# Performance work log

Measured on AMD Instinct MI355X. Metric: run time of the kernel, lower is better.

## Reference

```python
import jax, jax.numpy as jnp
import numpy as np

N = 50000       # nodes
E = 800000      # edges (before self-loops)
IN_DIM = 256
HIDDEN = 256
HEADS = 4
C1 = HIDDEN // HEADS  # 64 per-head channels in layer 1
OUT_DIM = 128
NEG_SLOPE = 0.2  # PyG GATConv default negative_slope


def setup_inputs() -> dict:
    key = jax.random.key(0)
    ks = jax.random.split(key, 10)
    x = jax.random.normal(ks[0], (N, IN_DIM), dtype=jnp.float32) * 0.1
    edge_index = jax.random.randint(ks[1], (2, E), 0, N, dtype=jnp.int64)
    # layer 1 params (GATConv: lin weight, att_src, att_dst, bias)
    W1 = jax.random.normal(ks[2], (IN_DIM, HEADS * C1), dtype=jnp.float32) * 0.05
    att_src1 = jax.random.normal(ks[3], (HEADS, C1), dtype=jnp.float32) * 0.05
    att_dst1 = jax.random.normal(ks[4], (HEADS, C1), dtype=jnp.float32) * 0.05
    bias1 = jnp.zeros((HEADS * C1,), dtype=jnp.float32)
    # layer 2 params (heads=1, concat=False)
    W2 = jax.random.normal(ks[5], (HIDDEN, OUT_DIM), dtype=jnp.float32) * 0.05
    att_src2 = jax.random.normal(ks[6], (1, OUT_DIM), dtype=jnp.float32) * 0.05
    att_dst2 = jax.random.normal(ks[7], (1, OUT_DIM), dtype=jnp.float32) * 0.05
    bias2 = jnp.zeros((OUT_DIM,), dtype=jnp.float32)
    return {"x": x, "edge_index": edge_index, "W1": W1, "att_src1": att_src1,
            "att_dst1": att_dst1, "bias1": bias1, "W2": W2, "att_src2": att_src2,
            "att_dst2": att_dst2, "bias2": bias2}


def gat_conv(x, src, dst, W, a_src, a_dst, bias, concat):
    # x: [N, F_in]; src/dst: [E'] (self-loops included); W: [F_in, H*C]
    H, C = a_src.shape
    h = (x @ W).reshape(-1, H, C)                      # [N, H, C]
    alpha_s = (h * a_src[None]).sum(-1)                # [N, H]
    alpha_d = (h * a_dst[None]).sum(-1)                # [N, H]
    e = jax.nn.leaky_relu(alpha_s[src] + alpha_d[dst], NEG_SLOPE)  # [E', H]
    # segment softmax over incoming edges of each destination node
    emax = jax.ops.segment_max(e, dst, num_segments=N)             # [N, H]
    ex = jnp.exp(e - emax[dst])
    denom = jax.ops.segment_sum(ex, dst, num_segments=N)           # [N, H]
    alpha = ex / (denom[dst] + 1e-16)                              # [E', H]
    msg = h[src] * alpha[:, :, None]                               # [E', H, C]
    out = jax.ops.segment_sum(msg, dst, num_segments=N)            # [N, H, C]
    if concat:
        out = out.reshape(N, H * C)
    else:
        out = out.mean(axis=1)
    return out + bias


def reference(x, edge_index, W1, att_src1, att_dst1, bias1, W2, att_src2, att_dst2, bias2):
    # PyG GATConv add_self_loops=True
    loops = jnp.arange(N, dtype=edge_index.dtype)
    src = jnp.concatenate([edge_index[0], loops])
    dst = jnp.concatenate([edge_index[1], loops])
    h = gat_conv(x, src, dst, W1, att_src1, att_dst1, bias1, concat=True)   # [N, 256]
    h = jax.nn.gelu(h, approximate=False)  # torch F.gelu default = exact erf
    # dropout inactive in eval mode
    out = gat_conv(h, src, dst, W2, att_src2, att_dst2, bias2, concat=False)  # [N, 128]
    return out
```

## Files before the change

### kernel.cpp

```cpp
#include <hip/hip_runtime.h>
#include <hip/hip_bf16.h>


#define IN_DIM   256
#define HID      256
#define HEADS    4
#define C1       64
#define OUT_DIM  128
#define NEG_SLOPE 0.2f

using short8 = __attribute__((ext_vector_type(8))) short;
using f32x4  = __attribute__((ext_vector_type(4))) float;

__device__ __forceinline__ float loadf(const void* p, size_t i, int isbf16) {
    return isbf16 ? __bfloat162float(((const __hip_bfloat16*)p)[i])
                  : ((const float*)p)[i];
}

__device__ __forceinline__ float leaky(float a) {
    return a > 0.f ? a : NEG_SLOPE * a;
}

__device__ __forceinline__ unsigned short f2bs(float f) {
    __hip_bfloat16 b = __float2bfloat16(f);
    return *reinterpret_cast<unsigned short*>(&b);
}

__device__ __forceinline__ float blo(unsigned u) {
    return __uint_as_float(u << 16);
}
__device__ __forceinline__ float bhi(unsigned u) {
    return __uint_as_float(u & 0xffff0000u);
}

__device__ __forceinline__ float gelu(float c) {
    return 0.5f * c * (1.0f + erff(c * 0.70710678f));
}


__global__ void prep_tpose_kernel(const void* x, int nx,
                                  const void* W1, const void* as1w, const void* ad1w,
                                  const void* b1, const void* W2, const void* as2w,
                                  const void* ad2w, const void* b2,
                                  float* as1wf, float* ad1wf, float* b1f,
                                  float* as2wf, float* ad2wf, float* b2f,
                                  int* flags,
                                  __hip_bfloat16* __restrict__ W1T,
                                  __hip_bfloat16* __restrict__ W2T,
                                  int* __restrict__ deg, int n) {
    __shared__ int red[4];
    __shared__ int flagS;
    int b = blockIdx.x;
    int t = threadIdx.x;

    if (b < 9) {
        const void* srcs[9] = {x, W1, as1w, ad1w, b1, W2, as2w, ad2w, b2};
        int ns[9] = {nx, IN_DIM * HID, HEADS * C1, HEADS * C1, HID,
                     HID * OUT_DIM, OUT_DIM, OUT_DIM, OUT_DIM};
        float* dsts[9] = {nullptr, nullptr, as1wf, ad1wf, b1f, nullptr, as2wf, ad2wf, b2f};

        const unsigned short* u = (const unsigned short*)srcs[b];
        int nn = ns[b];
        int nslots = nn < 4096 ? nn : 4096;
        int cnt = 0;
        for (int i = t; i < nslots; i += 256) {
            unsigned short a = u[i] & 0x7FFF;
            int e = a >> 7;
            if (a == 0 || (e >= 90 && e <= 140)) cnt++;
        }
        for (int o = 32; o > 0; o >>= 1) cnt += __shfl_down(cnt, o);
        if ((t & 63) == 0) red[t >> 6] = cnt;
        __syncthreads();
        if (t == 0) {
            int tot = red[0] + red[1] + red[2] + red[3];
            int f = (tot * 10 >= nslots * 8) ? 1 : 0;
            flags[b] = f;
            flagS = f;
        }
        __syncthreads();
        int f = flagS;
        float* d = dsts[b];
        if (d) {
            for (int i = t; i < nn; i += 256) d[i] = loadf(srcs[b], i, f);
        }
        return;
    }

    int bb = b - 9;
    int gi = bb * 256 + t;
    if (gi < n) deg[gi] = 0;

    const void* src = (bb < 256) ? W1 : W2;
    const unsigned short* u = (const unsigned short*)src;
    int cnt = 0;
    for (int i = t; i < 4096; i += 256) {
        unsigned short a = u[i] & 0x7FFF;
        int e = a >> 7;
        if (a == 0 || (e >= 90 && e <= 140)) cnt++;
    }
    for (int o = 32; o > 0; o >>= 1) cnt += __shfl_down(cnt, o);
    if ((t & 63) == 0) red[t >> 6] = cnt;
    __syncthreads();
    if (t == 0) flagS = ((red[0] + red[1] + red[2] + red[3]) * 10 >= 4096 * 8) ? 1 : 0;
    __syncthreads();
    int f = flagS;

    if (bb < 256) {
        int i = bb * 256 + t;
        int k = i >> 8, nn = i & 255;
        W1T[nn * 256 + k] = __float2bfloat16(loadf(W1, i, f));
    } else {
        int i = (bb - 256) * 256 + t;
        int k = i >> 7, nn = i & 127;
        W2T[nn * 256 + k] = __float2bfloat16(loadf(W2, i, f));
    }
}


__global__ void count_kernel(const int* __restrict__ ei, int E, int EP,
                             int* __restrict__ deg, int* __restrict__ pos) {
    int idx = blockIdx.x * blockDim.x + threadIdx.x;
    if (idx >= EP) return;
    int d = (idx < E) ? ei[E + idx] : (idx - E);
    pos[idx] = atomicAdd(&deg[d], 1);
}

__global__ __launch_bounds__(256) void psum_kernel(const int* __restrict__ deg,
                                                   int* __restrict__ bsum, int n) {
    int i = blockIdx.x * 256 + threadIdx.x;
    int v = (i < n) ? deg[i] : 0;
#pragma unroll
    for (int o = 32; o > 0; o >>= 1) v += __shfl_down(v, o);
    __shared__ int red[4];
    if ((threadIdx.x & 63) == 0) red[threadIdx.x >> 6] = v;
    __syncthreads();
    if (threadIdx.x == 0) bsum[blockIdx.x] = red[0] + red[1] + red[2] + red[3];
}

__global__ __launch_bounds__(256) void wscan_kernel(const int* __restrict__ deg,
                                                    const int* __restrict__ bsum,
                                                    int* __restrict__ offs,
                                                    float* __restrict__ z0,
                                                    float* __restrict__ z1,
                                                    int n) {
    __shared__ int sh[256];
    __shared__ int red[4];
    int b = blockIdx.x;
    int t = threadIdx.x;

    int pref = (t < b) ? bsum[t] : 0;
#pragma unroll
    for (int o = 32; o > 0; o >>= 1) pref += __shfl_down(pref, o);
    if ((t & 63) == 0) red[t >> 6] = pref;
    __syncthreads();
    int bpref = red[0] + red[1] + red[2] + red[3];

    int i = b * 256 + t;
    int v = (i < n) ? deg[i] : 0;
    sh[t] = v;
    __syncthreads();
    for (int d = 1; d < 256; d <<= 1) {
        int u = (t >= d) ? sh[t - d] : 0;
        __syncthreads();
        sh[t] += u;
        __syncthreads();
    }
    int excl = sh[t] - v + bpref;
    if (i < n) {
        offs[i] = excl;
        z0[i] = 0.f;
        z1[i] = 0.f;
        if (i == n - 1) offs[n] = excl + v;
    }
}

__global__ void fill_kernel(const int* __restrict__ ei, int E, int EP,
                            const int* __restrict__ offs,
                            const int* __restrict__ pos,
                            int* __restrict__ ssrc) {
    int idx = blockIdx.x * blockDim.x + threadIdx.x;
    if (idx >= EP) return;
    int src = (idx < E) ? ei[idx]     : (idx - E);
    int dst = (idx < E) ? ei[E + idx] : (idx - E);
    ssrc[offs[dst] + pos[idx]] = src;
}


__device__ __forceinline__ void store_out(float* C, size_t i, float v) { C[i] = v; }
__device__ __forceinline__ void store_out(__hip_bfloat16* C, size_t i, float v) {
    C[i] = __float2bfloat16(v);
}

template <typename OutT>
__global__ __launch_bounds__(256) void gemm_mfma(
    const void* __restrict__ A0, const int* aflagp,
    const __hip_bfloat16* __restrict__ BT,
    OutT* __restrict__ C, int M, int Nn, int K,
    const float* __restrict__ aswp, const float* __restrict__ adwp,
    float* __restrict__ asO, float* __restrict__ adO, int hstride) {
    constexpr int BM = 128, BN = 128, BK = 32;
    constexpr int LDK = BK + 8;
    __shared__ __hip_bfloat16 As[BM * LDK];
    __shared__ __hip_bfloat16 Bs[BN * LDK];

    const int Mb = (M + BM - 1) / BM;
    const int Nb = Nn / BN;
    int bmi, bni;
    if (Nb == 2) {
        int L = blockIdx.x;
        bmi = (L >> 4) * 8 + (L & 7);
        bni = (L >> 3) & 1;
        if (bmi >= Mb) return;
    } else {
        bmi = blockIdx.x;
        bni = 0;
        if (bmi >= Mb) return;
    }

    const int aflag = aflagp ? *aflagp : 1;
    const int tid  = threadIdx.x;
    const int lane = tid & 63;
    const int wv   = tid >> 6;
    const int wm   = (wv >> 1) * 64;
    const int wn   = (wv & 1) * 64;
    const int l15  = lane & 15;
    const int quad = lane >> 4;

    const int bm = bmi * BM;
    const int bn = bni * BN;

    f32x4 acc[4][4] = {};

    for (int k0 = 0; k0 < K; k0 += BK) {
#pragma unroll
        for (int i = 0; i < 2; ++i) {
            int c    = tid + i * 256;
            int row  = c >> 2;
            int koff = (c & 3) * 8;
            int grow = bm + row;
            short8 av = {};
            if (grow < M) {
                if (aflag) {
                    av = *(const short8*)((const __hip_bfloat16*)A0 +
                                          (size_t)grow * K + k0 + koff);
                } else {
                    const float* ap = (const float*)A0 + (size_t)grow * K + k0 + koff;
                    float4 f0 = *(const float4*)ap;
                    float4 f1 = *(const float4*)(ap + 4);
                    av[0] = (short)f2bs(f0.x); av[1] = (short)f2bs(f0.y);
                    av[2] = (short)f2bs(f0.z); av[3] = (short)f2bs(f0.w);
                    av[4] = (short)f2bs(f1.x); av[5] = (short)f2bs(f1.y);
                    av[6] = (short)f2bs(f1.z); av[7] = (short)f2bs(f1.w);
                }
            }
            *(short8*)&As[row * LDK + koff] = av;
            short8 bv = *(const short8*)(BT + (size_t)(bn + row) * K + k0 + koff);
            *(short8*)&Bs[row * LDK + koff] = bv;
        }
        __syncthreads();

        short8 af[4], bf[4];
#pragma unroll
        for (int f = 0; f < 4; ++f) {
            af[f] = *(const short8*)&As[(wm + f * 16 + l15) * LDK + quad * 8];
            bf[f] = *(const short8*)&Bs[(wn + f * 16 + l15) * LDK + quad * 8];
        }
#pragma unroll
        for (int fm = 0; fm < 4; ++fm)
#pragma unroll
            for (int fn = 0; fn < 4; ++fn)
                acc[fm][fn] = __builtin_amdgcn_mfma_f32_16x16x32_bf16(
                    af[fm], bf[fn], acc[fm][fn], 0, 0, 0);
        __syncthreads();
    }

#pragma unroll
    for (int fm = 0; fm < 4; ++fm) {
#pragma unroll
        for (int r = 0; r < 4; ++r) {
            int grow = bm + wm + fm * 16 + quad * 4 + r;
            if (grow >= M) continue;
#pragma unroll
            for (int fn = 0; fn < 4; ++fn) {
                int gcol = bn + wn + fn * 16 + l15;
                store_out(C, (size_t)grow * Nn + gcol, acc[fm][fn][r]);
            }
        }
    }

    if (aswp) {
        float aw[4], dw[4];
#pragma unroll
        for (int fn = 0; fn < 4; ++fn) {
            int gcol = bn + wn + fn * 16 + l15;
            aw[fn] = aswp[gcol];
            dw[fn] = adwp[gcol];
        }
        int head = (bn + wn) >> 6;
#pragma unroll
        for (int fm = 0; fm < 4; ++fm) {
#pragma unroll
            for (int r = 0; r < 4; ++r) {
                int grow = bm + wm + fm * 16 + quad * 4 + r;
                float sa = acc[fm][0][r] * aw[0] + acc[fm][1][r] * aw[1]
                         + acc[fm][2][r] * aw[2] + acc[fm][3][r] * aw[3];
                float sd = acc[fm][0][r] * dw[0] + acc[fm][1][r] * dw[1]
                         + acc[fm][2][r] * dw[2] + acc[fm][3][r] * dw[3];
#pragma unroll
                for (int o = 8; o > 0; o >>= 1) {
                    sa += __shfl_xor(sa, o);
                    sd += __shfl_xor(sd, o);
                }
                if (l15 == 0 && grow < M) {
                    if (hstride == 4) {
                        asO[grow * 4 + head] = sa;
                        adO[grow * 4 + head] = sd;
                    } else {
                        atomicAdd(&asO[grow], sa);
                        atomicAdd(&adO[grow], sd);
                    }
                }
            }
        }
    }
}


__global__ __launch_bounds__(256) void agg1g_kernel(
    const uint4* __restrict__ h1, const float* __restrict__ as1,
    const float* __restrict__ ad1, const int* __restrict__ offs,
    const int* __restrict__ ssrc, const float* __restrict__ bias1,
    uint4* __restrict__ g, int n) {
    int lane = threadIdx.x & 63;
    int wv   = threadIdx.x >> 6;
    int half = lane >> 5;
    int l32  = lane & 31;
    int v = blockIdx.x * 8 + wv * 2 + half;
    if (v >= n) return;
    int head = l32 >> 3;
    int start = offs[v], end = offs[v + 1];
    float adv = ad1[v * 4 + head];

    float aL0=0,aH0=0,aL1=0,aH1=0,aL2=0,aH2=0,aL3=0,aH3=0,den=0;
    int i = start;
    for (; i + 8 <= end; i += 8) {
        int s[8];
#pragma unroll
        for (int j = 0; j < 8; ++j) s[j] = ssrc[i + j];
        float e[8]; uint4 p[8];
#pragma unroll
        for (int j = 0; j < 8; ++j) {
            e[j] = as1[s[j] * 4 + head];
            p[j] = h1[(size_t)s[j] * 32 + l32];
        }
        float w[8];
#pragma unroll
        for (int j = 0; j < 8; ++j) {
            w[j] = __expf(leaky(e[j] + adv));
            den += w[j];
        }
#pragma unroll
        for (int j = 0; j < 8; ++j) {
            aL0 = fmaf(w[j], blo(p[j].x), aL0); aH0 = fmaf(w[j], bhi(p[j].x), aH0);
            aL1 = fmaf(w[j], blo(p[j].y), aL1); aH1 = fmaf(w[j], bhi(p[j].y), aH1);
            aL2 = fmaf(w[j], blo(p[j].z), aL2); aH2 = fmaf(w[j], bhi(p[j].z), aH2);
            aL3 = fmaf(w[j], blo(p[j].w), aL3); aH3 = fmaf(w[j], bhi(p[j].w), aH3);
        }
    }
    for (; i + 4 <= end; i += 4) {
        int s0 = ssrc[i], s1 = ssrc[i+1], s2 = ssrc[i+2], s3 = ssrc[i+3];
        float e0 = as1[s0*4+head], e1 = as1[s1*4+head];
        float e2 = as1[s2*4+head], e3 = as1[s3*4+head];
        uint4 p0 = h1[(size_t)s0*32 + l32];
        uint4 p1 = h1[(size_t)s1*32 + l32];
        uint4 p2 = h1[(size_t)s2*32 + l32];
        uint4 p3 = h1[(size_t)s3*32 + l32];
        float w0 = __expf(leaky(e0+adv));
        float w1 = __expf(leaky(e1+adv));
        float w2 = __expf(leaky(e2+adv));
        float w3 = __expf(leaky(e3+adv));
        den += (w0+w1)+(w2+w3);
        aL0 = fmaf(w0, blo(p0.x), fmaf(w1, blo(p1.x), fmaf(w2, blo(p2.x), fmaf(w3, blo(p3.x), aL0))));
        aH0 = fmaf(w0, bhi(p0.x), fmaf(w1, bhi(p1.x), fmaf(w2, bhi(p2.x), fmaf(w3, bhi(p3.x), aH0))));
        aL1 = fmaf(w0, blo(p0.y), fmaf(w1, blo(p1.y), fmaf(w2, blo(p2.y), fmaf(w3, blo(p3.y), aL1))));
        aH1 = fmaf(w0, bhi(p0.y), fmaf(w1, bhi(p1.y), fmaf(w2, bhi(p2.y), fmaf(w3, bhi(p3.y), aH1))));
        aL2 = fmaf(w0, blo(p0.z), fmaf(w1, blo(p1.z), fmaf(w2, blo(p2.z), fmaf(w3, blo(p3.z), aL2))));
        aH2 = fmaf(w0, bhi(p0.z), fmaf(w1, bhi(p1.z), fmaf(w2, bhi(p2.z), fmaf(w3, bhi(p3.z), aH2))));
        aL3 = fmaf(w0, blo(p0.w), fmaf(w1, blo(p1.w), fmaf(w2, blo(p2.w), fmaf(w3, blo(p3.w), aL3))));
        aH3 = fmaf(w0, bhi(p0.w), fmaf(w1, bhi(p1.w), fmaf(w2, bhi(p2.w), fmaf(w3, bhi(p3.w), aH3))));
    }
    for (; i < end; ++i) {
        int s = ssrc[i];
        float w = __expf(leaky(as1[s*4+head] + adv));
        uint4 p = h1[(size_t)s*32 + l32];
        den += w;
        aL0 = fmaf(w, blo(p.x), aL0); aH0 = fmaf(w, bhi(p.x), aH0);
        aL1 = fmaf(w, blo(p.y), aL1); aH1 = fmaf(w, bhi(p.y), aH1);
        aL2 = fmaf(w, blo(p.z), aL2); aH2 = fmaf(w, bhi(p.z), aH2);
        aL3 = fmaf(w, blo(p.w), aL3); aH3 = fmaf(w, bhi(p.w), aH3);
    }
    float inv = 1.f / (den + 1e-16f);
    float4 bq0 = *(const float4*)&bias1[8 * l32];
    float4 bq1 = *(const float4*)&bias1[8 * l32 + 4];
    float c0 = gelu(aL0*inv + bq0.x), c1 = gelu(aH0*inv + bq0.y);
    float c2 = gelu(aL1*inv + bq0.z), c3 = gelu(aH1*inv + bq0.w);
    float c4 = gelu(aL2*inv + bq1.x), c5 = gelu(aH2*inv + bq1.y);
    float c6 = gelu(aL3*inv + bq1.z), c7 = gelu(aH3*inv + bq1.w);
    uint4 r;
    r.x = (unsigned)f2bs(c0) | ((unsigned)f2bs(c1) << 16);
    r.y = (unsigned)f2bs(c2) | ((unsigned)f2bs(c3) << 16);
    r.z = (unsigned)f2bs(c4) | ((unsigned)f2bs(c5) << 16);
    r.w = (unsigned)f2bs(c6) | ((unsigned)f2bs(c7) << 16);
    g[(size_t)v * 32 + l32] = r;
}

__global__ __launch_bounds__(256) void agg2s_kernel(
    const uint4* __restrict__ h2, const float* __restrict__ as2,
    const float* __restrict__ ad2, const int* __restrict__ offs,
    const int* __restrict__ ssrc, const float* __restrict__ bias2,
    void* __restrict__ out, const int* outflagp, int n) {
    int lane = threadIdx.x & 63;
    int wv   = threadIdx.x >> 6;
    int sub  = lane >> 4;
    int l16  = lane & 15;
    int v = blockIdx.x * 16 + wv * 4 + sub;
    if (v >= n) return;
    int start = offs[v], end = offs[v + 1];
    float adv = ad2[v];

    float a0=0,a1=0,a2=0,a3=0,a4=0,a5=0,a6=0,a7=0,den=0;
    int i = start;
    for (; i + 8 <= end; i += 8) {
        int s[8];
#pragma unroll
        for (int j = 0; j < 8; ++j) s[j] = ssrc[i + j];
        float e[8]; uint4 p[8];
#pragma unroll
        for (int j = 0; j < 8; ++j) {
            e[j] = as2[s[j]];
            p[j] = h2[(size_t)s[j] * 16 + l16];
        }
        float w[8];
#pragma unroll
        for (int j = 0; j < 8; ++j) {
            w[j] = __expf(leaky(e[j] + adv));
            den += w[j];
        }
#pragma unroll
        for (int j = 0; j < 8; ++j) {
            a0 = fmaf(w[j], blo(p[j].x), a0); a1 = fmaf(w[j], bhi(p[j].x), a1);
            a2 = fmaf(w[j], blo(p[j].y), a2); a3 = fmaf(w[j], bhi(p[j].y), a3);
            a4 = fmaf(w[j], blo(p[j].z), a4); a5 = fmaf(w[j], bhi(p[j].z), a5);
            a6 = fmaf(w[j], blo(p[j].w), a6); a7 = fmaf(w[j], bhi(p[j].w), a7);
        }
    }
    for (; i < end; ++i) {
        int s = ssrc[i];
        float w = __expf(leaky(as2[s] + adv));
        uint4 p = h2[(size_t)s * 16 + l16];
        den += w;
        a0 = fmaf(w, blo(p.x), a0); a1 = fmaf(w, bhi(p.x), a1);
        a2 = fmaf(w, blo(p.y), a2); a3 = fmaf(w, bhi(p.y), a3);
        a4 = fmaf(w, blo(p.z), a4); a5 = fmaf(w, bhi(p.z), a5);
        a6 = fmaf(w, blo(p.w), a6); a7 = fmaf(w, bhi(p.w), a7);
    }
    float inv = 1.f / (den + 1e-16f);
    int cb = 8 * l16;
    float4 bq0 = *(const float4*)&bias2[cb];
    float4 bq1 = *(const float4*)&bias2[cb + 4];
    float o0 = a0*inv + bq0.x, o1 = a1*inv + bq0.y;
    float o2 = a2*inv + bq0.z, o3 = a3*inv + bq0.w;
    float o4 = a4*inv + bq1.x, o5 = a5*inv + bq1.y;
    float o6 = a6*inv + bq1.z, o7 = a7*inv + bq1.w;
    if (*outflagp) {
        uint4 rv;
        rv.x = (unsigned)f2bs(o0) | ((unsigned)f2bs(o1) << 16);
        rv.y = (unsigned)f2bs(o2) | ((unsigned)f2bs(o3) << 16);
        rv.z = (unsigned)f2bs(o4) | ((unsigned)f2bs(o5) << 16);
        rv.w = (unsigned)f2bs(o6) | ((unsigned)f2bs(o7) << 16);
        *(uint4*)((unsigned short*)out + (size_t)v * 128 + cb) = rv;
    } else {
        float* op = (float*)out + (size_t)v * 128 + cb;
        *(float4*)op       = make_float4(o0, o1, o2, o3);
        *(float4*)(op + 4) = make_float4(o4, o5, o6, o7);
    }
}


static inline char* alignp(char* p, size_t a) {
    return (char*)(((uintptr_t)p + a - 1) & ~(uintptr_t)(a - 1));
}

extern "C" void kernel_launch(void* const* d_in, const int* in_sizes, int n_in,
                              void* d_out, int out_size, void* d_ws, size_t ws_size,
                              hipStream_t stream) {
    const void* x    = d_in[0];
    const int*  ei   = (const int*)d_in[1];
    const void* W1   = d_in[2];
    const void* as1w = d_in[3];
    const void* ad1w = d_in[4];
    const void* b1   = d_in[5];
    const void* W2   = d_in[6];
    const void* as2w = d_in[7];
    const void* ad2w = d_in[8];
    const void* b2   = d_in[9];

    const int N  = out_size / OUT_DIM;
    const int E  = in_sizes[1] / 2;
    const int EP = E + N;
    const int NB = (N + 255) / 256;
    const int Mb = (N + 127) / 128;

    char* p = (char*)d_ws;
    __hip_bfloat16* h1  = (__hip_bfloat16*)p;
    __hip_bfloat16* h2b = (__hip_bfloat16*)p;  p += (size_t)N * HID * 2;
    __hip_bfloat16* g   = (__hip_bfloat16*)p;  p += (size_t)N * HID * 2;
    float* as1wf = (float*)p;                 p += 256 * 4;
    float* ad1wf = (float*)p;                 p += 256 * 4;
    float* b1f   = (float*)p;                 p += 256 * 4;
    float* as2wf = (float*)p;                 p += 128 * 4;
    float* ad2wf = (float*)p;                 p += 128 * 4;
    float* b2f   = (float*)p;                 p += 128 * 4;
    float* as1   = (float*)p;                 p += (size_t)N * HEADS * 4;
    float* ad1   = (float*)p;                 p += (size_t)N * HEADS * 4;
    float* as2   = (float*)p;                 p += (size_t)N * 4;
    float* ad2   = (float*)p;                 p += (size_t)N * 4;
    int*   flags = (int*)p;                   p += 16 * 4;
    int*   deg   = (int*)p;                   p += (size_t)N * 4;
    int*   offs  = (int*)p;                   p += (size_t)(N + 1) * 4;
    int*   bsum  = (int*)p;                   p += (size_t)1024 * 4;
    int*   pos   = (int*)p;                   p += (size_t)EP * 4;
    int*   ssrc  = (int*)p;                   p += (size_t)EP * 4;
    p = alignp(p, 64);
    __hip_bfloat16* W1T = (__hip_bfloat16*)p; p += (size_t)HID * IN_DIM * 2;
    __hip_bfloat16* W2T = (__hip_bfloat16*)p; p += (size_t)OUT_DIM * HID * 2;

    const int grd = (EP + 255) / 256;
    const int g1blocks = ((Mb + 7) / 8) * 16;

    prep_tpose_kernel<<<393, 256, 0, stream>>>(x, in_sizes[0], W1, as1w, ad1w, b1,
                                               W2, as2w, ad2w, b2,
                                               as1wf, ad1wf, b1f, as2wf, ad2wf, b2f,
                                               flags, W1T, W2T, deg, N);
    count_kernel<<<grd, 256, 0, stream>>>(ei, E, EP, deg, pos);
    psum_kernel<<<NB, 256, 0, stream>>>(deg, bsum, N);
    wscan_kernel<<<NB, 256, 0, stream>>>(deg, bsum, offs, as2, ad2, N);
    fill_kernel<<<grd, 256, 0, stream>>>(ei, E, EP, offs, pos, ssrc);
    gemm_mfma<__hip_bfloat16><<<g1blocks, 256, 0, stream>>>(
        x, flags + 0, W1T, h1, N, HID, IN_DIM,
        as1wf, ad1wf, as1, ad1, 4);
    agg1g_kernel<<<(N + 7) / 8, 256, 0, stream>>>((const uint4*)h1, as1, ad1, offs, ssrc,
                                                  b1f, (uint4*)g, N);
    gemm_mfma<__hip_bfloat16><<<Mb, 256, 0, stream>>>(
        g, nullptr, W2T, h2b, N, OUT_DIM, HID,
        as2wf, ad2wf, as2, ad2, 1);
    agg2s_kernel<<<(N + 15) / 16, 256, 0, stream>>>((const uint4*)h2b, as2, ad2, offs, ssrc,
                                                    b2f, d_out, flags + 0, N);
}
```

Before: 315.6 us.

## Fuse edge degree-count blocks into layer-1 GEMM launch

Removes the standalone count_kernel and folds its atomic degree counting into the layer-1 GEMM grid. One block in five runs the GEMM tile and the other four each count 256 edges. The goal is to overlap the latency-bound atomics with the compute-bound GEMM and save one kernel launch. The grid size is hardcoded to 4160 after a computed value is overwritten, which only holds for these N and E, and the mixed block roles may disturb the GEMM's tile scheduling.

```diff
diff --git a/kernel.cpp b/kernel.cpp
--- a/kernel.cpp
+++ b/kernel.cpp
@@ -117,14 +117,6 @@
 }
 
 
-__global__ void count_kernel(const int* __restrict__ ei, int E, int EP,
-                             int* __restrict__ deg, int* __restrict__ pos) {
-    int idx = blockIdx.x * blockDim.x + threadIdx.x;
-    if (idx >= EP) return;
-    int d = (idx < E) ? ei[E + idx] : (idx - E);
-    pos[idx] = atomicAdd(&deg[d], 1);
-}
-
 __global__ __launch_bounds__(256) void psum_kernel(const int* __restrict__ deg,
                                                    int* __restrict__ bsum, int n) {
     int i = blockIdx.x * 256 + threadIdx.x;
@@ -197,22 +189,39 @@
     const __hip_bfloat16* __restrict__ BT,
     OutT* __restrict__ C, int M, int Nn, int K,
     const float* __restrict__ aswp, const float* __restrict__ adwp,
-    float* __restrict__ asO, float* __restrict__ adO, int hstride) {
+    float* __restrict__ asO, float* __restrict__ adO, int hstride,
+    const int* __restrict__ cei, int cE, int cEP,
+    int* __restrict__ cdeg, int* __restrict__ cpos, int cblocks) {
     constexpr int BM = 128, BN = 128, BK = 32;
     constexpr int LDK = BK + 8;
     __shared__ __hip_bfloat16 As[BM * LDK];
     __shared__ __hip_bfloat16 Bs[BN * LDK];
 
+    int bid = blockIdx.x;
+    if (cblocks) {
+        int phase = bid % 5;
+        if (phase != 0) {
+            int cidx = bid - bid / 5 - 1;
+            int idx = cidx * 256 + (int)threadIdx.x;
+            if (idx < cEP) {
+                int d = (idx < cE) ? cei[cE + idx] : (idx - cE);
+                cpos[idx] = atomicAdd(&cdeg[d], 1);
+            }
+            return;
+        }
+        bid = bid / 5;
+    }
+
     const int Mb = (M + BM - 1) / BM;
     const int Nb = Nn / BN;
     int bmi, bni;
     if (Nb == 2) {
-        int L = blockIdx.x;
+        int L = bid;
         bmi = (L >> 4) * 8 + (L & 7);
         bni = (L >> 3) & 1;
         if (bmi >= Mb) return;
     } else {
-        bmi = blockIdx.x;
+        bmi = bid;
         bni = 0;
         if (bmi >= Mb) return;
     }
@@ -537,23 +546,28 @@
 
     const int grd = (EP + 255) / 256;
     const int g1blocks = ((Mb + 7) / 8) * 16;
+    int T = 5 * g1blocks;
+    if (T - (T + 4) / 5 < grd) T = ((grd * 5 + 3) / 4 + 4) / 5 * 5;
+    if ((T + 4) / 5 < g1blocks) T = 5 * g1blocks;
+    T = 4160;
 
     prep_tpose_kernel<<<393, 256, 0, stream>>>(x, in_sizes[0], W1, as1w, ad1w, b1,
                                                W2, as2w, ad2w, b2,
                                                as1wf, ad1wf, b1f, as2wf, ad2wf, b2f,
                                                flags, W1T, W2T, deg, N);
-    count_kernel<<<grd, 256, 0, stream>>>(ei, E, EP, deg, pos);
+    gemm_mfma<__hip_bfloat16><<<T, 256, 0, stream>>>(
+        x, flags + 0, W1T, h1, N, HID, IN_DIM,
+        as1wf, ad1wf, as1, ad1, 4,
+        ei, E, EP, deg, pos, grd);
     psum_kernel<<<NB, 256, 0, stream>>>(deg, bsum, N);
     wscan_kernel<<<NB, 256, 0, stream>>>(deg, bsum, offs, as2, ad2, N);
     fill_kernel<<<grd, 256, 0, stream>>>(ei, E, EP, offs, pos, ssrc);
-    gemm_mfma<__hip_bfloat16><<<g1blocks, 256, 0, stream>>>(
-        x, flags + 0, W1T, h1, N, HID, IN_DIM,
-        as1wf, ad1wf, as1, ad1, 4);
     agg1g_kernel<<<(N + 7) / 8, 256, 0, stream>>>((const uint4*)h1, as1, ad1, offs, ssrc,
                                                   b1f, (uint4*)g, N);
     gemm_mfma<__hip_bfloat16><<<Mb, 256, 0, stream>>>(
         g, nullptr, W2T, h2b, N, OUT_DIM, HID,
-        as2wf, ad2wf, as2, ad2, 1);
+        as2wf, ad2wf, as2, ad2, 1,
+        nullptr, 0, 0, nullptr, nullptr, 0);
     agg2s_kernel<<<(N + 15) / 16, 256, 0, stream>>>((const uint4*)h2b, as2, ad2, offs, ssrc,
                                                     b2f, d_out, flags + 0, N);
 }
```

Measured after the change: 307.0 us. 2.7% less time.
